# Kernel optimization log

Measured on AMD Instinct MI355X. Metric: run time of the kernel, lower is better.

The kernel has to match this reference:

```python
import jax, jax.numpy as jnp
import numpy as np

SIGMA_YX = 0.09
SIGMA_HW = 0.3


def setup_inputs() -> dict:
    key = jax.random.key(0)
    k1, k2 = jax.random.split(key)
    B, T, D = 16, 1024, 256
    z = jax.random.normal(k1, (B, T, D), dtype=jnp.float32)
    z = z / jnp.linalg.norm(z, axis=-1, keepdims=True)  # L2-normalized per docstring
    # small normalized offsets so the Gaussian kernel is non-degenerate
    gt_dT = 0.1 * jax.random.normal(k2, (B, T, T, 4), dtype=jnp.float32)
    return {"z": z, "gt_dT": gt_dT}


def reference(z, gt_dT):
    # sigma2 buffer: [sigma_yx^2, sigma_yx^2, sigma_hw^2, sigma_hw^2]
    sigma2 = jnp.array([SIGMA_YX**2, SIGMA_YX**2, SIGMA_HW**2, SIGMA_HW**2],
                       dtype=gt_dT.dtype)
    # RBF affinity: w[b,t,s] = exp(-sum_k dT^2 / (2 sigma2))  -> (B,T,T)
    w = jnp.exp(-jnp.sum(gt_dT * gt_dT / (2.0 * sigma2), axis=-1))
    # Laplacian energy tr(Z^T L Z), L = D - W
    d = w.sum(-1)                                   # (B,T) degree
    z2 = jnp.sum(z * z, axis=-1)                    # (B,T)
    wz = jnp.einsum('bts,bsd->btd', w, z)           # (B,T,D)
    term1 = jnp.sum(z2 * d, axis=-1)                # (B,)
    term2 = 2.0 * jnp.sum(wz * z, axis=(-1, -2))    # (B,)
    term3 = jnp.sum(z2[:, None, :] * w, axis=(-1, -2))  # (B,)
    num = term1 - term2 + term3
    denom = jnp.maximum(w.sum(axis=(-1, -2)), 1e-6)
    return jnp.mean(num / denom)
```

## Files before the change

kernel.cpp:

```cpp
#include <hip/hip_runtime.h>
#include <hip/hip_bf16.h>

#define BB 16
#define TT 1024
#define DD 256
#define BM 64
#define BN 64
#define LDK 264

typedef __attribute__((ext_vector_type(4))) float f32x4;
typedef __bf16 bf16x8 __attribute__((ext_vector_type(8)));

__global__ void zero_ws_kernel(float* ws) {
    if (threadIdx.x < 2 * BB) ws[threadIdx.x] = 0.0f;
}

__global__ __launch_bounds__(256, 2) void psl_main(
    const float* __restrict__ z, const float* __restrict__ gt,
    float* __restrict__ accum) {
    __shared__ __hip_bfloat16 As[BM * LDK];
    __shared__ __hip_bfloat16 Bs[BN * LDK];
    __shared__ float z2t[BM];
    __shared__ float z2s[BN];
    __shared__ float rbuf[8];

    const int tid  = threadIdx.x;
    const int lane = tid & 63;
    const int wv   = tid >> 6;
    const int b    = blockIdx.z;
    const int t0   = blockIdx.y * BM;
    const int s0   = blockIdx.x * BN;

    for (int half = 0; half < 2; ++half) {
        const int base       = half ? s0 : t0;
        __hip_bfloat16* dst  = half ? Bs : As;
        float* z2dst         = half ? z2s : z2t;
        for (int pass = 0; pass < 16; ++pass) {
            const int row = pass * 4 + wv;
            const f32x4 v = reinterpret_cast<const f32x4*>(
                z + ((size_t)b * TT + base + row) * DD)[lane];
            __hip_bfloat16 h0 = __float2bfloat16(v.x);
            __hip_bfloat16 h1 = __float2bfloat16(v.y);
            __hip_bfloat16 h2 = __float2bfloat16(v.z);
            __hip_bfloat16 h3 = __float2bfloat16(v.w);
            ushort4 pk;
            pk.x = *reinterpret_cast<const unsigned short*>(&h0);
            pk.y = *reinterpret_cast<const unsigned short*>(&h1);
            pk.z = *reinterpret_cast<const unsigned short*>(&h2);
            pk.w = *reinterpret_cast<const unsigned short*>(&h3);
            *reinterpret_cast<ushort4*>(&dst[row * LDK + lane * 4]) = pk;
            float ss = v.x * v.x + v.y * v.y + v.z * v.z + v.w * v.w;
            #pragma unroll
            for (int off = 32; off; off >>= 1) ss += __shfl_xor(ss, off);
            if (lane == 0) z2dst[row] = ss;
        }
    }
    __syncthreads();

    const int lane15 = lane & 15;
    const int quad   = lane >> 4;

    f32x4 acc[4];
    #pragma unroll
    for (int j = 0; j < 4; ++j) acc[j] = (f32x4){0.f, 0.f, 0.f, 0.f};

    const __hip_bfloat16* Abase = As + (wv * 16 + lane15) * LDK + quad * 8;
    const __hip_bfloat16* Bbase = Bs + lane15 * LDK + quad * 8;
    #pragma unroll
    for (int kk = 0; kk < 8; ++kk) {
        bf16x8 af = *reinterpret_cast<const bf16x8*>(Abase + kk * 32);
        #pragma unroll
        for (int j = 0; j < 4; ++j) {
            bf16x8 bfj = *reinterpret_cast<const bf16x8*>(Bbase + j * 16 * LDK + kk * 32);
            acc[j] = __builtin_amdgcn_mfma_f32_16x16x32_bf16(af, bfj, acc[j], 0, 0, 0);
        }
    }

    const float c_yx = 1.0f / (2.0f * 0.09f * 0.09f);
    const float c_hw = 1.0f / (2.0f * 0.3f * 0.3f);
    const int trow0 = wv * 16 + quad * 4;
    float z2t_r[4];
    #pragma unroll
    for (int i = 0; i < 4; ++i) z2t_r[i] = z2t[trow0 + i];

    float nsum = 0.0f, dsum = 0.0f;
    #pragma unroll
    for (int j = 0; j < 4; ++j) {
        const int s_loc = j * 16 + lane15;
        const float z2s_r = z2s[s_loc];
        const f32x4* gp = reinterpret_cast<const f32x4*>(gt)
                        + (((size_t)b * TT + t0 + trow0) * TT + s0 + s_loc);
        #pragma unroll
        for (int i = 0; i < 4; ++i) {
            const f32x4 dv = gp[(size_t)i * TT];
            const float e = (dv.x * dv.x + dv.y * dv.y) * c_yx
                          + (dv.z * dv.z + dv.w * dv.w) * c_hw;
            const float wgt = __expf(-e);
            nsum += wgt * (z2t_r[i] + z2s_r - 2.0f * acc[j][i]);
            dsum += wgt;
        }
    }

    #pragma unroll
    for (int off = 32; off; off >>= 1) {
        nsum += __shfl_xor(nsum, off);
        dsum += __shfl_xor(dsum, off);
    }
    if (lane == 0) { rbuf[wv] = nsum; rbuf[4 + wv] = dsum; }
    __syncthreads();
    if (tid == 0) {
        const float n = rbuf[0] + rbuf[1] + rbuf[2] + rbuf[3];
        const float d = rbuf[4] + rbuf[5] + rbuf[6] + rbuf[7];
        atomicAdd(&accum[b], n);
        atomicAdd(&accum[BB + b], d);
    }
}

__global__ void finalize_kernel(const float* __restrict__ accum,
                                float* __restrict__ out) {
    if (threadIdx.x == 0 && blockIdx.x == 0) {
        float s = 0.0f;
        for (int b = 0; b < BB; ++b)
            s += accum[b] / fmaxf(accum[BB + b], 1e-6f);
        out[0] = s / (float)BB;
    }
}

extern "C" void kernel_launch(void* const* d_in, const int* in_sizes, int n_in,
                              void* d_out, int out_size, void* d_ws, size_t ws_size,
                              hipStream_t stream) {
    const float* z  = (const float*)d_in[0];
    const float* gt = (const float*)d_in[1];
    float* out   = (float*)d_out;
    float* accum = (float*)d_ws;

    zero_ws_kernel<<<1, 64, 0, stream>>>(accum);
    dim3 grid(TT / BN, TT / BM, BB);
    psl_main<<<grid, 256, 0, stream>>>(z, gt, accum);
    finalize_kernel<<<1, 64, 0, stream>>>(accum, out);
}
```

Measured before the change: 474.9 us.

## Precompute bf16 MFMA fragments and row norms in global memory, drop LDS staging

Adds separate kernels that compute per-row squared norms and convert z into bf16 in the exact MFMA fragment order once. The main kernel then loads its operands straight from global memory into registers instead of re-converting z and staging it in shared memory in every tile. This removes the LDS footprint, the barrier, and the redundant fp32 loads and conversions, and raises the occupancy target to 4 blocks per CU. In exchange it adds two extra launches and relies on L2 reuse of the fragment buffer.

```diff
diff --git a/kernel.cpp b/kernel.cpp
--- a/kernel.cpp
+++ b/kernel.cpp
@@ -6,22 +6,62 @@
 #define DD 256
 #define BM 64
 #define BN 64
-#define LDK 264
+#define NGRP 64
+#define NKK 8
 
 typedef __attribute__((ext_vector_type(4))) float f32x4;
 typedef __bf16 bf16x8 __attribute__((ext_vector_type(8)));
+typedef unsigned short u16;
+typedef u16 u16x8 __attribute__((ext_vector_type(8)));
 
-__global__ void zero_ws_kernel(float* ws) {
-    if (threadIdx.x < 2 * BB) ws[threadIdx.x] = 0.0f;
+#define WS_Z2_OFF   8388608
+#define WS_ACC_OFF  8454144
+
+__global__ void zero_accum_kernel(float* acc) {
+    if (threadIdx.x < 2 * BB) acc[threadIdx.x] = 0.0f;
 }
 
-__global__ __launch_bounds__(256, 2) void psl_main(
-    const float* __restrict__ z, const float* __restrict__ gt,
-    float* __restrict__ accum) {
-    __shared__ __hip_bfloat16 As[BM * LDK];
-    __shared__ __hip_bfloat16 Bs[BN * LDK];
-    __shared__ float z2t[BM];
-    __shared__ float z2s[BN];
+__global__ __launch_bounds__(256) void z2_kernel(
+    const float* __restrict__ z, float* __restrict__ z2g) {
+    const int lane = threadIdx.x & 63;
+    const int wv   = threadIdx.x >> 6;
+    const int row  = blockIdx.x * 4 + wv;
+    const f32x4 v = reinterpret_cast<const f32x4*>(z + (size_t)row * DD)[lane];
+    float ss = v.x * v.x + v.y * v.y + v.z * v.z + v.w * v.w;
+    #pragma unroll
+    for (int off = 32; off; off >>= 1) ss += __shfl_xor(ss, off);
+    if (lane == 0) z2g[row] = ss;
+}
+
+__global__ __launch_bounds__(256) void frag_kernel(
+    const float* __restrict__ z, u16* __restrict__ zf) {
+    const int lane = threadIdx.x & 63;
+    const int wv   = threadIdx.x >> 6;
+    const int wid  = blockIdx.x * 4 + wv;
+    const int b    = wid >> 9;
+    const int rem  = wid & 511;
+    const int g    = rem >> 3;
+    const int kk   = rem & 7;
+    const int lane15 = lane & 15;
+    const int quad   = lane >> 4;
+
+    const float* src = z + (((size_t)b * TT + g * 16 + lane15) * DD
+                            + kk * 32 + quad * 8);
+    const f32x4 v0 = reinterpret_cast<const f32x4*>(src)[0];
+    const f32x4 v1 = reinterpret_cast<const f32x4*>(src)[1];
+    float f[8] = {v0.x, v0.y, v0.z, v0.w, v1.x, v1.y, v1.z, v1.w};
+    u16x8 pk;
+    #pragma unroll
+    for (int e = 0; e < 8; ++e) {
+        __hip_bfloat16 h = __float2bfloat16(f[e]);
+        pk[e] = *reinterpret_cast<const u16*>(&h);
+    }
+    reinterpret_cast<u16x8*>(zf)[(size_t)wid * 64 + lane] = pk;
+}
+
+__global__ __launch_bounds__(256, 4) void psl_main(
+    const u16* __restrict__ zf, const float* __restrict__ z2g,
+    const float* __restrict__ gt, float* __restrict__ accum) {
     __shared__ float rbuf[8];
 
     const int tid  = threadIdx.x;
@@ -30,49 +70,29 @@
     const int b    = blockIdx.z;
     const int t0   = blockIdx.y * BM;
     const int s0   = blockIdx.x * BN;
-
-    for (int half = 0; half < 2; ++half) {
-        const int base       = half ? s0 : t0;
-        __hip_bfloat16* dst  = half ? Bs : As;
-        float* z2dst         = half ? z2s : z2t;
-        for (int pass = 0; pass < 16; ++pass) {
-            const int row = pass * 4 + wv;
-            const f32x4 v = reinterpret_cast<const f32x4*>(
-                z + ((size_t)b * TT + base + row) * DD)[lane];
-            __hip_bfloat16 h0 = __float2bfloat16(v.x);
-            __hip_bfloat16 h1 = __float2bfloat16(v.y);
-            __hip_bfloat16 h2 = __float2bfloat16(v.z);
-            __hip_bfloat16 h3 = __float2bfloat16(v.w);
-            ushort4 pk;
-            pk.x = *reinterpret_cast<const unsigned short*>(&h0);
-            pk.y = *reinterpret_cast<const unsigned short*>(&h1);
-            pk.z = *reinterpret_cast<const unsigned short*>(&h2);
-            pk.w = *reinterpret_cast<const unsigned short*>(&h3);
-            *reinterpret_cast<ushort4*>(&dst[row * LDK + lane * 4]) = pk;
-            float ss = v.x * v.x + v.y * v.y + v.z * v.z + v.w * v.w;
-            #pragma unroll
-            for (int off = 32; off; off >>= 1) ss += __shfl_xor(ss, off);
-            if (lane == 0) z2dst[row] = ss;
-        }
-    }
-    __syncthreads();
-
     const int lane15 = lane & 15;
     const int quad   = lane >> 4;
+
+    const bf16x8* fragp = reinterpret_cast<const bf16x8*>(zf);
+    const int gA = blockIdx.y * 4 + wv;
+    const int gB0 = blockIdx.x * 4;
+
+    bf16x8 af[8];
+    #pragma unroll
+    for (int kk = 0; kk < NKK; ++kk)
+        af[kk] = fragp[(((size_t)b * NGRP + gA) * NKK + kk) * 64 + lane];
 
     f32x4 acc[4];
     #pragma unroll
     for (int j = 0; j < 4; ++j) acc[j] = (f32x4){0.f, 0.f, 0.f, 0.f};
 
-    const __hip_bfloat16* Abase = As + (wv * 16 + lane15) * LDK + quad * 8;
-    const __hip_bfloat16* Bbase = Bs + lane15 * LDK + quad * 8;
     #pragma unroll
-    for (int kk = 0; kk < 8; ++kk) {
-        bf16x8 af = *reinterpret_cast<const bf16x8*>(Abase + kk * 32);
+    for (int j = 0; j < 4; ++j) {
+        const size_t bbase = ((size_t)b * NGRP + gB0 + j) * NKK;
         #pragma unroll
-        for (int j = 0; j < 4; ++j) {
-            bf16x8 bfj = *reinterpret_cast<const bf16x8*>(Bbase + j * 16 * LDK + kk * 32);
-            acc[j] = __builtin_amdgcn_mfma_f32_16x16x32_bf16(af, bfj, acc[j], 0, 0, 0);
+        for (int kk = 0; kk < NKK; ++kk) {
+            bf16x8 bfj = fragp[(bbase + kk) * 64 + lane];
+            acc[j] = __builtin_amdgcn_mfma_f32_16x16x32_bf16(af[kk], bfj, acc[j], 0, 0, 0);
         }
     }
 
@@ -81,13 +101,13 @@
     const int trow0 = wv * 16 + quad * 4;
     float z2t_r[4];
     #pragma unroll
-    for (int i = 0; i < 4; ++i) z2t_r[i] = z2t[trow0 + i];
+    for (int i = 0; i < 4; ++i) z2t_r[i] = z2g[b * TT + t0 + trow0 + i];
 
     float nsum = 0.0f, dsum = 0.0f;
     #pragma unroll
     for (int j = 0; j < 4; ++j) {
         const int s_loc = j * 16 + lane15;
-        const float z2s_r = z2s[s_loc];
+        const float z2s_r = z2g[b * TT + s0 + s_loc];
         const f32x4* gp = reinterpret_cast<const f32x4*>(gt)
                         + (((size_t)b * TT + t0 + trow0) * TT + s0 + s_loc);
         #pragma unroll
@@ -131,11 +151,17 @@
                               hipStream_t stream) {
     const float* z  = (const float*)d_in[0];
     const float* gt = (const float*)d_in[1];
-    float* out   = (float*)d_out;
-    float* accum = (float*)d_ws;
+    float* out = (float*)d_out;
 
-    zero_ws_kernel<<<1, 64, 0, stream>>>(accum);
+    char* ws = (char*)d_ws;
+    u16*   zf    = (u16*)ws;
+    float* z2g   = (float*)(ws + WS_Z2_OFF);
+    float* accum = (float*)(ws + WS_ACC_OFF);
+
+    zero_accum_kernel<<<1, 64, 0, stream>>>(accum);
+    z2_kernel<<<BB * TT / 4, 256, 0, stream>>>(z, z2g);
+    frag_kernel<<<BB * NGRP * NKK / 4, 256, 0, stream>>>(z, zf);
     dim3 grid(TT / BN, TT / BM, BB);
-    psl_main<<<grid, 256, 0, stream>>>(z, gt, accum);
+    psl_main<<<grid, 256, 0, stream>>>(zf, z2g, gt, accum);
     finalize_kernel<<<1, 64, 0, stream>>>(accum, out);
 }
```

Result: faster. 382.4 us (-19.5%).
